# Kernel tuning notes

Hardware: AMD Instinct MI355X
Metric: run time of the kernel (lower is better)

Reference implementation:

```python
import jax, jax.numpy as jnp
import numpy as np

# Module config (matches init_kwargs)
N_HEADS = 16
HEAD = 64
SEQ = 4096          # single prefill sequence (cu_seqlens_k = [0, SEQ])
BS = 64             # block_size (both q and k blocks)
LOCAL = 8           # local_blocks
VERT = 8            # vert_stride
NB = SEQ // BS      # number of blocks along seq
SLIDE = max(1, VERT // N_HEADS)  # get_head_sliding_step(16, 8, homo_head=False) -> 1
SM_SCALE = 1.0 / float(np.sqrt(HEAD))


def _build_layout():
    """Per-head block-sparse layout: causal + (local OR strided-vertical) blocks,
    padded to a fixed max nnz per row (CSR rows -> padded col indices + valid mask)."""
    h = np.arange(N_HEADS)[:, None, None]
    i = np.arange(NB)[None, :, None]
    j = np.arange(NB)[None, None, :]
    mask = (j <= i) & (((i - j) < LOCAL) | (((j + h * SLIDE + 1) % VERT) == 0))
    max_nnz = int(mask.sum(-1).max())
    cols = np.zeros((N_HEADS, NB, max_nnz), np.int32)
    valid = np.zeros((N_HEADS, NB, max_nnz), bool)
    for hh in range(N_HEADS):
        for ii in range(NB):
            c = np.nonzero(mask[hh, ii])[0]
            cols[hh, ii, :len(c)] = c
            valid[hh, ii, :len(c)] = True
    return cols, valid, max_nnz

_COLS_NP, _VALID_NP, MAX_NNZ = _build_layout()
COLS = jnp.asarray(_COLS_NP)    # [H, NB, NNZ] k-block ids (padded with 0)
VALID = jnp.asarray(_VALID_NP)  # [H, NB, NNZ] padding mask


def setup_inputs() -> dict:
    key = jax.random.key(0)
    kq, kk, kv = jax.random.split(key, 3)
    q = jax.random.normal(kq, (SEQ, N_HEADS, HEAD), jnp.float32)
    k = jax.random.normal(kk, (SEQ, N_HEADS, HEAD), jnp.float32)
    v = jax.random.normal(kv, (SEQ, N_HEADS, HEAD), jnp.float32)
    cu_seqlens_k = jnp.array([0, SEQ], jnp.int32)
    return {"q": q, "k": k, "v": v, "cu_seqlens_k": cu_seqlens_k}


def _attn(q, k, v):
    # [T, H, D] -> [H, NB, BS, D]
    qb = q.transpose(1, 0, 2).reshape(N_HEADS, NB, BS, HEAD)
    kb = k.transpose(1, 0, 2).reshape(N_HEADS, NB, BS, HEAD)
    vb = v.transpose(1, 0, 2).reshape(N_HEADS, NB, BS, HEAD)
    gather = jax.vmap(lambda x, c: x[c])  # per-head block gather
    kg = gather(kb, COLS)  # [H, NB, NNZ, BS, D]
    vg = gather(vb, COLS)  # [H, NB, NNZ, BS, D]
    # block-sparse scores: [H, NB(q blk), BS(m), NNZ(n), BS(j)]
    scores = jnp.einsum('himd,hinjd->himnj', qb, kg) * SM_SCALE
    qpos = jnp.arange(NB)[:, None] * BS + jnp.arange(BS)[None, :]   # [NB, BS]
    kpos = COLS[..., None] * BS + jnp.arange(BS)                    # [H, NB, NNZ, BS]
    allow = VALID[:, :, None, :, None] & (
        qpos[None, :, :, None, None] >= kpos[:, :, None, :, :])
    scores = jnp.where(allow, scores, -jnp.inf)
    p = jax.nn.softmax(scores.reshape(N_HEADS, NB, BS, MAX_NNZ * BS), axis=-1)
    p = p.reshape(N_HEADS, NB, BS, MAX_NNZ, BS)
    out = jnp.einsum('himnj,hinjd->himd', p, vg)
    return out.reshape(N_HEADS, SEQ, HEAD).transpose(1, 0, 2)  # [T, H, D]


def reference(q, k, v, cu_seqlens_k):
    # single-sequence prefill: past_len = 0, q_len == k_len == SEQ
    return _attn(q, k, v)
```

## Files before the change

### kernel.cpp

```cpp
#include <hip/hip_runtime.h>
#include <hip/hip_bf16.h>
#include <math.h>


#define NHEADS 16
#define HDIM   64
#define NBLK   64
#define SEQLEN 4096
#define KP     72
#define SMAX   16.0f

typedef __attribute__((ext_vector_type(8))) short bf16x8;
typedef __attribute__((ext_vector_type(4))) float f32x4;

__device__ __forceinline__ short f2bf(float x) {
    union { float f; unsigned u; } c; c.f = x;
    unsigned u = c.u;
    return (short)((u + 0x7FFFu + ((u >> 16) & 1u)) >> 16);
}
__device__ __forceinline__ short f2bf_trunc(float x) {
    union { float f; unsigned u; } c; c.f = x;
    return (short)(c.u >> 16);
}

__device__ __forceinline__ void load_lds16(const short* g, const short* l) {
    __builtin_amdgcn_global_load_lds(
        (const __attribute__((address_space(1))) void*)g,
        (__attribute__((address_space(3))) void*)l, 16, 0, 0);
}

__global__ __launch_bounds__(256)
void prep_kernel(const float* __restrict__ k, const float* __restrict__ v,
                 short* __restrict__ kt, short* __restrict__ vt) {
    __shared__ short tile[64 * KP];
    const int b = blockIdx.x;
    const int h = b >> 6, jb = b & 63;
    const int tid = threadIdx.x;

    #pragma unroll
    for (int it = 0; it < 4; ++it) {
        int e = it * 1024 + tid * 4;
        int key = e >> 6, d0 = e & 63;
        float4 f = *(const float4*)(v + ((size_t)(jb * 64 + key) * NHEADS + h) * HDIM + d0);
        tile[(d0 + 0) * KP + key] = f2bf(f.x);
        tile[(d0 + 1) * KP + key] = f2bf(f.y);
        tile[(d0 + 2) * KP + key] = f2bf(f.z);
        tile[(d0 + 3) * KP + key] = f2bf(f.w);
    }
    __syncthreads();
    short* vtile = vt + (size_t)b * 4096;
    #pragma unroll
    for (int ii = 0; ii < 2; ++ii) {
        int idx = ii * 256 + tid;
        int d = idx >> 3, gsw = idx & 7;
        int g = gsw ^ (d & 7);
        bf16x8 val = *(const bf16x8*)&tile[d * KP + g * 8];
        *(bf16x8*)(vtile + (size_t)idx * 8) = val;
    }
    short* ktile = kt + (size_t)b * 4096;
    #pragma unroll
    for (int ii = 0; ii < 2; ++ii) {
        int idx = ii * 256 + tid;
        int r = idx >> 3, g = idx & 7;
        const float* src = k + ((size_t)(jb * 64 + r) * NHEADS + h) * HDIM + g * 8;
        float4 f0 = *(const float4*)src;
        float4 f1 = *(const float4*)(src + 4);
        bf16x8 a;
        a[0]=f2bf(f0.x); a[1]=f2bf(f0.y); a[2]=f2bf(f0.z); a[3]=f2bf(f0.w);
        a[4]=f2bf(f1.x); a[5]=f2bf(f1.y); a[6]=f2bf(f1.z); a[7]=f2bf(f1.w);
        int G = r * 8 + (g ^ (r & 7));
        *(bf16x8*)(ktile + (size_t)G * 8) = a;
    }
}

__global__ __launch_bounds__(512, 4)
void attn_kernel(const short* __restrict__ kt, const short* __restrict__ vt,
                 const float* __restrict__ q, float* __restrict__ out) {
    __shared__ short kv[2 * 8192];
    __shared__ short pl[8 * 1024];

    const int b    = blockIdx.x;
    const int h    = ((b & 7) << 1) | ((b >> 3) & 1);
    const int g5   = b >> 4;
    const int m    = (g5 < 16) ? g5 : (47 - g5);
    const int q0   = 2 * m, q1 = 2 * m + 1;
    const int tid  = threadIdx.x;
    const int wave = tid >> 6;
    const int lane = tid & 63;
    const int l16  = lane & 15;
    const int quad = lane >> 4;

    const int myqi   = q0 + (wave >> 2);
    const int stripe = wave & 3;
    const int row0   = myqi * 64 + stripe * 16;
    short* pw = pl + wave * 1024;

    const float* qrow = q + ((size_t)(row0 + l16) * NHEADS + h) * HDIM;
    bf16x8 a_q[2];
    #pragma unroll
    for (int kk = 0; kk < 2; ++kk) {
        const float* src = qrow + kk * 32 + quad * 8;
        float4 f0 = *(const float4*)(src);
        float4 f1 = *(const float4*)(src + 4);
        bf16x8 a;
        a[0]=f2bf(f0.x); a[1]=f2bf(f0.y); a[2]=f2bf(f0.z); a[3]=f2bf(f0.w);
        a[4]=f2bf(f1.x); a[5]=f2bf(f1.y); a[6]=f2bf(f1.z); a[7]=f2bf(f1.w);
        a_q[kk] = a;
    }

    f32x4 o[4];
    float lsum[4];
    #pragma unroll
    for (int nt = 0; nt < 4; ++nt) { o[nt] = (f32x4){0.f,0.f,0.f,0.f}; lsum[nt] = 0.f; }

    const short* kth = kt + (size_t)(h * 64) * 4096;
    const short* vth = vt + (size_t)(h * 64) * 4096;
    const float kscale = 0.125f * 1.4426950408889634f;

    const int j0  = (7 - h) & 7;
    const int l0  = (q0 > 7) ? (q0 - 7) : 0;
    const int nv  = (j0 < l0) ? ((l0 - j0 + 7) >> 3) : 0;
    const int T   = nv + (q1 - l0 + 1);

    const int r7   = l16 & 7;
    const int gk0  = (quad ^ r7) * 8;
    const int gk1  = gk0 ^ 32;
    const int rowb = l16 * 64;
    const int pr0  = rowb + (((  quad) ^ r7) << 3);
    const int pr1  = rowb + (((4 + quad) ^ r7) << 3);

    {
        const short* ktb = kth + (size_t)((0 < nv) ? j0 : l0) * 4096;
        const short* vtb = vth + (size_t)((0 < nv) ? j0 : l0) * 4096;
        load_lds16(ktb + (size_t)tid * 8, &kv[wave * 512]);
        load_lds16(vtb + (size_t)tid * 8, &kv[4096 + wave * 512]);
    }

    for (int t = 0; t < T; ++t) {
        const int jb = (t < nv) ? (j0 + 8 * t) : (l0 + (t - nv));

        __syncthreads();

        if (t + 1 < T) {
            const int jn = (t + 1 < nv) ? (j0 + 8 * (t + 1)) : (l0 + (t + 1 - nv));
            const int bo = ((t + 1) & 1) * 8192;
            const short* ktb = kth + (size_t)jn * 4096;
            const short* vtb = vth + (size_t)jn * 4096;
            load_lds16(ktb + (size_t)tid * 8, &kv[bo + wave * 512]);
            load_lds16(vtb + (size_t)tid * 8, &kv[bo + 4096 + wave * 512]);
        }

        const bool part = (jb <= myqi) &&
                          (((myqi - jb) < 8) || (((jb + h + 1) & 7) == 0));
        if (part) {
            const short* kb = &kv[(t & 1) * 8192];
            const short* vb = kb + 4096;

            f32x4 s[4];
            #pragma unroll
            for (int nt = 0; nt < 4; ++nt) {
                bf16x8 k0 = *(const bf16x8*)&kb[nt * 1024 + rowb + gk0];
                bf16x8 k1 = *(const bf16x8*)&kb[nt * 1024 + rowb + gk1];
                s[nt] = (f32x4){0.f,0.f,0.f,0.f};
                s[nt] = __builtin_amdgcn_mfma_f32_16x16x32_bf16(a_q[0], k0, s[nt], 0, 0, 0);
                s[nt] = __builtin_amdgcn_mfma_f32_16x16x32_bf16(a_q[1], k1, s[nt], 0, 0, 0);
            }

            const bool diag = (jb == myqi);
            #pragma unroll
            for (int nt = 0; nt < 4; ++nt) {
                const int gw = nt * 2 + (l16 >> 3);
                const int ow = l16 & 7;
                #pragma unroll
                for (int r = 0; r < 4; ++r) {
                    float raw = s[nt][r];
                    const int mrow = stripe * 16 + quad * 4 + r;
                    if (diag) {
                        int n = nt * 16 + l16;
                        if (n > mrow) raw = -INFINITY;
                    }
                    float pv = __builtin_amdgcn_exp2f(fmaf(raw, kscale, -SMAX));
                    lsum[r] += pv;
                    const int prow = quad * 4 + r;
                    pw[prow * 64 + ((gw ^ (prow & 7)) << 3) + ow] = f2bf_trunc(pv);
                }
            }

            bf16x8 a_p0 = *(const bf16x8*)&pw[pr0];
            bf16x8 a_p1 = *(const bf16x8*)&pw[pr1];

            #pragma unroll
            for (int nt = 0; nt < 4; ++nt) {
                bf16x8 v0 = *(const bf16x8*)&vb[nt * 1024 + rowb + gk0];
                bf16x8 v1 = *(const bf16x8*)&vb[nt * 1024 + rowb + gk1];
                o[nt] = __builtin_amdgcn_mfma_f32_16x16x32_bf16(a_p0, v0, o[nt], 0, 0, 0);
                o[nt] = __builtin_amdgcn_mfma_f32_16x16x32_bf16(a_p1, v1, o[nt], 0, 0, 0);
            }
        }
    }

    #pragma unroll
    for (int r = 0; r < 4; ++r) {
        float tsum = lsum[r];
        #pragma unroll
        for (int off = 1; off < 16; off <<= 1)
            tsum += __shfl_xor(tsum, off);
        float inv = 1.0f / tsum;
        int trow = row0 + quad * 4 + r;
        float* orow = out + ((size_t)trow * NHEADS + h) * HDIM;
        #pragma unroll
        for (int nt = 0; nt < 4; ++nt)
            orow[nt * 16 + l16] = o[nt][r] * inv;
    }
}

extern "C" void kernel_launch(void* const* d_in, const int* in_sizes, int n_in,
                              void* d_out, int out_size, void* d_ws, size_t ws_size,
                              hipStream_t stream) {
    const float* q = (const float*)d_in[0];
    const float* k = (const float*)d_in[1];
    const float* v = (const float*)d_in[2];
    float* out = (float*)d_out;

    const size_t tileBytes = (size_t)NHEADS * NBLK * 4096 * sizeof(short);
    short* kt = (short*)d_ws;
    short* vt = (short*)((char*)d_ws + tileBytes);
    prep_kernel<<<dim3(NHEADS * NBLK), dim3(256), 0, stream>>>(k, v, kt, vt);
    attn_kernel<<<dim3(512), dim3(512), 0, stream>>>(kt, vt, q, out);
}
```

Before: 118.4 us.

## Process two KV blocks per barrier with four-stage LDS ring buffer

Grows the K/V LDS staging area from two to four slots and handles two key blocks between each __syncthreads, prefetching the next pair while computing the current pair. This halves the number of block-wide barriers and deepens the prefetch distance so more load latency can be hidden. In exchange, per-block LDS use rises from about 48KB to 80KB, which can lower the number of resident workgroups per CU relative to the launch-bounds hint of 4.

Measured after the change: 119.1 us. About the same (+0.5%).

```diff
diff --git a/kernel.cpp b/kernel.cpp
--- a/kernel.cpp
+++ b/kernel.cpp
@@ -76,7 +76,7 @@
 __global__ __launch_bounds__(512, 4)
 void attn_kernel(const short* __restrict__ kt, const short* __restrict__ vt,
                  const float* __restrict__ q, float* __restrict__ out) {
-    __shared__ short kv[2 * 8192];
+    __shared__ short kv[4 * 8192];
     __shared__ short pl[8 * 1024];
 
     const int b    = blockIdx.x;
@@ -126,34 +126,45 @@
     const int gk0  = (quad ^ r7) * 8;
     const int gk1  = gk0 ^ 32;
     const int rowb = l16 * 64;
-    const int pr0  = rowb + (((  quad) ^ r7) << 3);
+    const int pr0  = rowb + ((quad ^ r7) << 3);
     const int pr1  = rowb + (((4 + quad) ^ r7) << 3);
 
-    {
-        const short* ktb = kth + (size_t)((0 < nv) ? j0 : l0) * 4096;
-        const short* vtb = vth + (size_t)((0 < nv) ? j0 : l0) * 4096;
-        load_lds16(ktb + (size_t)tid * 8, &kv[wave * 512]);
-        load_lds16(vtb + (size_t)tid * 8, &kv[4096 + wave * 512]);
-    }
-
-    for (int t = 0; t < T; ++t) {
-        const int jb = (t < nv) ? (j0 + 8 * t) : (l0 + (t - nv));
-
+    #pragma unroll
+    for (int u = 0; u < 2; ++u) {
+        if (u < T) {
+            const int jb = (u < nv) ? (j0 + 8 * u) : (l0 + (u - nv));
+            const int so = u * 8192;
+            load_lds16(kth + (size_t)jb * 4096 + (size_t)tid * 8, &kv[so + wave * 512]);
+            load_lds16(vth + (size_t)jb * 4096 + (size_t)tid * 8, &kv[so + 4096 + wave * 512]);
+        }
+    }
+
+    const int MT = (T + 1) >> 1;
+    for (int Mi = 0; Mi < MT; ++Mi) {
         __syncthreads();
 
-        if (t + 1 < T) {
-            const int jn = (t + 1 < nv) ? (j0 + 8 * (t + 1)) : (l0 + (t + 1 - nv));
-            const int bo = ((t + 1) & 1) * 8192;
-            const short* ktb = kth + (size_t)jn * 4096;
-            const short* vtb = vth + (size_t)jn * 4096;
-            load_lds16(ktb + (size_t)tid * 8, &kv[bo + wave * 512]);
-            load_lds16(vtb + (size_t)tid * 8, &kv[bo + 4096 + wave * 512]);
+        #pragma unroll
+        for (int du = 2; du < 4; ++du) {
+            const int u = 2 * Mi + du;
+            if (u < T) {
+                const int jn = (u < nv) ? (j0 + 8 * u) : (l0 + (u - nv));
+                const int so = (u & 3) * 8192;
+                load_lds16(kth + (size_t)jn * 4096 + (size_t)tid * 8, &kv[so + wave * 512]);
+                load_lds16(vth + (size_t)jn * 4096 + (size_t)tid * 8, &kv[so + 4096 + wave * 512]);
+            }
         }
 
-        const bool part = (jb <= myqi) &&
-                          (((myqi - jb) < 8) || (((jb + h + 1) & 7) == 0));
-        if (part) {
-            const short* kb = &kv[(t & 1) * 8192];
+        #pragma unroll
+        for (int du = 0; du < 2; ++du) {
+            const int u = 2 * Mi + du;
+            if (u >= T) break;
+            const int jb = (u < nv) ? (j0 + 8 * u) : (l0 + (u - nv));
+
+            const bool part = (jb <= myqi) &&
+                              (((myqi - jb) < 8) || (((jb + h + 1) & 7) == 0));
+            if (!part) continue;
+
+            const short* kb = &kv[(u & 3) * 8192];
             const short* vb = kb + 4096;
 
             f32x4 s[4];
```

## Split attention into one q-block per workgroup and vectorize V transpose stores

Applied to the files above, without the earlier changes.

The attention kernel now gives each workgroup a single query block with 4 waves, instead of a pair of query blocks with 8 waves. The grid doubles to 1024 blocks, and the per-wave participation test that left half the waves idle on non-shared key blocks is removed, since every loaded key block is now needed. Query blocks are interleaved light/heavy to balance causal work across the grid. The cost is that each workgroup fetches its own K/V tiles, so the K/V reuse across two query blocks is lost. The prep kernel's V transpose now loads four keys per thread and writes short4 vectors to LDS instead of scalar stores.

New measurement: 120.2 us. Within noise of the previous version (+1.5%).

```diff
diff --git a/kernel.cpp b/kernel.cpp
--- a/kernel.cpp
+++ b/kernel.cpp
@@ -37,15 +37,22 @@
     const int h = b >> 6, jb = b & 63;
     const int tid = threadIdx.x;
 
-    #pragma unroll
-    for (int it = 0; it < 4; ++it) {
-        int e = it * 1024 + tid * 4;
-        int key = e >> 6, d0 = e & 63;
-        float4 f = *(const float4*)(v + ((size_t)(jb * 64 + key) * NHEADS + h) * HDIM + d0);
-        tile[(d0 + 0) * KP + key] = f2bf(f.x);
-        tile[(d0 + 1) * KP + key] = f2bf(f.y);
-        tile[(d0 + 2) * KP + key] = f2bf(f.z);
-        tile[(d0 + 3) * KP + key] = f2bf(f.w);
+    {
+        const int kg = tid >> 4;
+        const int dg = tid & 15;
+        float4 f[4];
+        #pragma unroll
+        for (int j = 0; j < 4; ++j)
+            f[j] = *(const float4*)(v + ((size_t)(jb * 64 + 4 * kg + j) * NHEADS + h) * HDIM + 4 * dg);
+        #pragma unroll
+        for (int i = 0; i < 4; ++i) {
+            short4 s4;
+            s4.x = f2bf(((const float*)&f[0])[i]);
+            s4.y = f2bf(((const float*)&f[1])[i]);
+            s4.z = f2bf(((const float*)&f[2])[i]);
+            s4.w = f2bf(((const float*)&f[3])[i]);
+            *(short4*)&tile[(4 * dg + i) * KP + 4 * kg] = s4;
+        }
     }
     __syncthreads();
     short* vtile = vt + (size_t)b * 4096;
@@ -73,26 +80,22 @@
     }
 }
 
-__global__ __launch_bounds__(512, 4)
+__global__ __launch_bounds__(256, 4)
 void attn_kernel(const short* __restrict__ kt, const short* __restrict__ vt,
                  const float* __restrict__ q, float* __restrict__ out) {
     __shared__ short kv[2 * 8192];
-    __shared__ short pl[8 * 1024];
+    __shared__ short pl[4 * 1024];
 
     const int b    = blockIdx.x;
     const int h    = ((b & 7) << 1) | ((b >> 3) & 1);
-    const int g5   = b >> 4;
-    const int m    = (g5 < 16) ? g5 : (47 - g5);
-    const int q0   = 2 * m, q1 = 2 * m + 1;
+    const int g6   = b >> 4;
+    const int qi   = (g6 & 1) ? (63 - (g6 >> 1)) : (g6 >> 1);
     const int tid  = threadIdx.x;
     const int wave = tid >> 6;
     const int lane = tid & 63;
     const int l16  = lane & 15;
     const int quad = lane >> 4;
-
-    const int myqi   = q0 + (wave >> 2);
-    const int stripe = wave & 3;
-    const int row0   = myqi * 64 + stripe * 16;
+    const int row0 = qi * 64 + wave * 16;
     short* pw = pl + wave * 1024;
 
     const float* qrow = q + ((size_t)(row0 + l16) * NHEADS + h) * HDIM;
@@ -118,84 +121,85 @@
     const float kscale = 0.125f * 1.4426950408889634f;
 
     const int j0  = (7 - h) & 7;
-    const int l0  = (q0 > 7) ? (q0 - 7) : 0;
-    const int nv  = (j0 < l0) ? ((l0 - j0 + 7) >> 3) : 0;
-    const int T   = nv + (q1 - l0 + 1);
-
-    const int r7   = l16 & 7;
-    const int gk0  = (quad ^ r7) * 8;
-    const int gk1  = gk0 ^ 32;
-    const int rowb = l16 * 64;
-    const int pr0  = rowb + (((  quad) ^ r7) << 3);
-    const int pr1  = rowb + (((4 + quad) ^ r7) << 3);
+    const int loc = (qi > 7) ? (qi - 7) : 0;
+    const int nv  = (j0 < loc) ? ((loc - j0 + 7) >> 3) : 0;
+    const int T   = nv + (qi - loc + 1);
+
+    const int sbase = wave * 64;
+    const int r7    = l16 & 7;
+    const int gk0   = (quad ^ r7) * 8;
+    const int gk1   = gk0 ^ 32;
+    const int rowb  = l16 * 64;
+    const int pr0   = rowb + ((quad ^ r7) << 3);
+    const int pr1   = rowb + (((4 + quad) ^ r7) << 3);
 
     {
-        const short* ktb = kth + (size_t)((0 < nv) ? j0 : l0) * 4096;
-        const short* vtb = vth + (size_t)((0 < nv) ? j0 : l0) * 4096;
-        load_lds16(ktb + (size_t)tid * 8, &kv[wave * 512]);
-        load_lds16(vtb + (size_t)tid * 8, &kv[4096 + wave * 512]);
+        const short* ktb = kth + (size_t)((0 < nv) ? j0 : loc) * 4096;
+        const short* vtb = vth + (size_t)((0 < nv) ? j0 : loc) * 4096;
+        load_lds16(ktb + (size_t)(sbase + lane) * 8,       &kv[sbase * 8]);
+        load_lds16(ktb + (size_t)(256 + sbase + lane) * 8, &kv[(256 + sbase) * 8]);
+        load_lds16(vtb + (size_t)(sbase + lane) * 8,       &kv[4096 + sbase * 8]);
+        load_lds16(vtb + (size_t)(256 + sbase + lane) * 8, &kv[4096 + (256 + sbase) * 8]);
     }
 
     for (int t = 0; t < T; ++t) {
-        const int jb = (t < nv) ? (j0 + 8 * t) : (l0 + (t - nv));
+        const int jb = (t < nv) ? (j0 + 8 * t) : (loc + (t - nv));
 
         __syncthreads();
 
         if (t + 1 < T) {
-            const int jn = (t + 1 < nv) ? (j0 + 8 * (t + 1)) : (l0 + (t + 1 - nv));
+            const int jn = (t + 1 < nv) ? (j0 + 8 * (t + 1)) : (loc + (t + 1 - nv));
             const int bo = ((t + 1) & 1) * 8192;
             const short* ktb = kth + (size_t)jn * 4096;
             const short* vtb = vth + (size_t)jn * 4096;
-            load_lds16(ktb + (size_t)tid * 8, &kv[bo + wave * 512]);
-            load_lds16(vtb + (size_t)tid * 8, &kv[bo + 4096 + wave * 512]);
-        }
-
-        const bool part = (jb <= myqi) &&
-                          (((myqi - jb) < 8) || (((jb + h + 1) & 7) == 0));
-        if (part) {
-            const short* kb = &kv[(t & 1) * 8192];
-            const short* vb = kb + 4096;
-
-            f32x4 s[4];
+            load_lds16(ktb + (size_t)(sbase + lane) * 8,       &kv[bo + sbase * 8]);
+            load_lds16(ktb + (size_t)(256 + sbase + lane) * 8, &kv[bo + (256 + sbase) * 8]);
+            load_lds16(vtb + (size_t)(sbase + lane) * 8,       &kv[bo + 4096 + sbase * 8]);
+            load_lds16(vtb + (size_t)(256 + sbase + lane) * 8, &kv[bo + 4096 + (256 + sbase) * 8]);
+        }
+
+        const short* kb = &kv[(t & 1) * 8192];
+        const short* vb = kb + 4096;
+
+        f32x4 s[4];
+        #pragma unroll
+        for (int nt = 0; nt < 4; ++nt) {
+            bf16x8 k0 = *(const bf16x8*)&kb[nt * 1024 + rowb + gk0];
+            bf16x8 k1 = *(const bf16x8*)&kb[nt * 1024 + rowb + gk1];
+            s[nt] = (f32x4){0.f,0.f,0.f,0.f};
+            s[nt] = __builtin_amdgcn_mfma_f32_16x16x32_bf16(a_q[0], k0, s[nt], 0, 0, 0);
+            s[nt] = __builtin_amdgcn_mfma_f32_16x16x32_bf16(a_q[1], k1, s[nt], 0, 0, 0);
+        }
+
+        const bool diag = (jb == qi);
+        #pragma unroll
+        for (int nt = 0; nt < 4; ++nt) {
+            const int gw = nt * 2 + (l16 >> 3);
+            const int ow = l16 & 7;
             #pragma unroll
-            for (int nt = 0; nt < 4; ++nt) {
-                bf16x8 k0 = *(const bf16x8*)&kb[nt * 1024 + rowb + gk0];
-                bf16x8 k1 = *(const bf16x8*)&kb[nt * 1024 + rowb + gk1];
-                s[nt] = (f32x4){0.f,0.f,0.f,0.f};
-                s[nt] = __builtin_amdgcn_mfma_f32_16x16x32_bf16(a_q[0], k0, s[nt], 0, 0, 0);
-                s[nt] = __builtin_amdgcn_mfma_f32_16x16x32_bf16(a_q[1], k1, s[nt], 0, 0, 0);
+            for (int r = 0; r < 4; ++r) {
+                float raw = s[nt][r];
+                if (diag) {
+                    int n = nt * 16 + l16;
+                    int mrow = wave * 16 + quad * 4 + r;
+                    if (n > mrow) raw = -INFINITY;
+                }
+                float pv = __builtin_amdgcn_exp2f(fmaf(raw, kscale, -SMAX));
+                lsum[r] += pv;
+                const int prow = quad * 4 + r;
+                pw[prow * 64 + ((gw ^ (prow & 7)) << 3) + ow] = f2bf_trunc(pv);
             }
-
-            const bool diag = (jb == myqi);
-            #pragma unroll
-            for (int nt = 0; nt < 4; ++nt) {
-                const int gw = nt * 2 + (l16 >> 3);
-                const int ow = l16 & 7;
-                #pragma unroll
-                for (int r = 0; r < 4; ++r) {
-                    float raw = s[nt][r];
-                    const int mrow = stripe * 16 + quad * 4 + r;
-                    if (diag) {
-                        int n = nt * 16 + l16;
-                        if (n > mrow) raw = -INFINITY;
-                    }
-                    float pv = __builtin_amdgcn_exp2f(fmaf(raw, kscale, -SMAX));
-                    lsum[r] += pv;
-                    const int prow = quad * 4 + r;
-                    pw[prow * 64 + ((gw ^ (prow & 7)) << 3) + ow] = f2bf_trunc(pv);
-                }
-            }
-
-            bf16x8 a_p0 = *(const bf16x8*)&pw[pr0];
-            bf16x8 a_p1 = *(const bf16x8*)&pw[pr1];
-
-            #pragma unroll
-            for (int nt = 0; nt < 4; ++nt) {
-                bf16x8 v0 = *(const bf16x8*)&vb[nt * 1024 + rowb + gk0];
-                bf16x8 v1 = *(const bf16x8*)&vb[nt * 1024 + rowb + gk1];
-                o[nt] = __builtin_amdgcn_mfma_f32_16x16x32_bf16(a_p0, v0, o[nt], 0, 0, 0);
-                o[nt] = __builtin_amdgcn_mfma_f32_16x16x32_bf16(a_p1, v1, o[nt], 0, 0, 0);
-            }
+        }
+
+        bf16x8 a_p0 = *(const bf16x8*)&pw[pr0];
+        bf16x8 a_p1 = *(const bf16x8*)&pw[pr1];
+
+        #pragma unroll
+        for (int nt = 0; nt < 4; ++nt) {
+            bf16x8 v0 = *(const bf16x8*)&vb[nt * 1024 + rowb + gk0];
+            bf16x8 v1 = *(const bf16x8*)&vb[nt * 1024 + rowb + gk1];
+            o[nt] = __builtin_amdgcn_mfma_f32_16x16x32_bf16(a_p0, v0, o[nt], 0, 0, 0);
+            o[nt] = __builtin_amdgcn_mfma_f32_16x16x32_bf16(a_p1, v1, o[nt], 0, 0, 0);
         }
     }
 
@@ -226,5 +230,5 @@
     short* kt = (short*)d_ws;
     short* vt = (short*)((char*)d_ws + tileBytes);
     prep_kernel<<<dim3(NHEADS * NBLK), dim3(256), 0, stream>>>(k, v, kt, vt);
-    attn_kernel<<<dim3(512), dim3(512), 0, stream>>>(kt, vt, q, out);
-}
+    attn_kernel<<<dim3(NHEADS * NBLK), dim3(256), 0, stream>>>(kt, vt, q, out);
+}
```
